# Performance work log

Measured on AMD Instinct MI355X. Metric: run time of the kernel, lower is better.

Reference implementation:

```python
import jax, jax.numpy as jnp
import numpy as np
from jax import lax

K = 31          # mip_kernel
P_LO, P_HI = 0.01, 0.99
ALPHA = 0.15
MU = 10.0
PD_ITERS = 30
TAU = 0.125
SIG = 0.125
THETA = 1.0
EPS = 1e-6


def _max_pool(x, k):
    # torch F.max_pool2d with stride=1, padding=k//2 pads with -inf
    p = k // 2
    return lax.reduce_window(
        x, -jnp.inf, lax.max,
        window_dimensions=(1, 1, k, k),
        window_strides=(1, 1, 1, 1),
        padding=[(0, 0), (0, 0), (p, p), (p, p)])


def _forward_grad(u):
    # forward differences, zero-padded on the far edge (same shape as u)
    dx = jnp.pad(u[..., :, 1:] - u[..., :, :-1], ((0, 0), (0, 0), (0, 0), (0, 1)))
    dy = jnp.pad(u[..., 1:, :] - u[..., :-1, :], ((0, 0), (0, 0), (0, 1), (0, 0)))
    return dx, dy


def _divergence(px, py):
    div_x = px - jnp.pad(px[..., :, :-1], ((0, 0), (0, 0), (0, 0), (1, 0)))
    div_y = py - jnp.pad(py[..., :-1, :], ((0, 0), (0, 0), (1, 0), (0, 0)))
    return div_x + div_y


def _robust_normalize(x):
    B = x.shape[0]
    flat = x.reshape(B, -1)
    lo = jnp.quantile(flat, P_LO, axis=1).reshape(B, 1, 1, 1)
    hi = jnp.quantile(flat, P_HI, axis=1).reshape(B, 1, 1, 1)
    return jnp.clip((x - lo) / (hi - lo + EPS), 0.0, 1.0)


def setup_inputs() -> dict:
    key = jax.random.key(0)
    Iy = jax.random.uniform(key, (16, 3, 512, 512), dtype=jnp.float32)
    return {"Iy": Iy}


def reference(Iy):
    B = Iy.shape[0]
    R, G, Bc = Iy[:, 0:1], Iy[:, 1:2], Iy[:, 2:3]

    Rmax = _max_pool(R, K)
    GBmax = jnp.maximum(_max_pool(G, K), _max_pool(Bc, K))
    Dmip_abs = jnp.abs(Rmax - GBmax)

    N_hat = _robust_normalize(Dmip_abs + R)

    dxh, dyh = _forward_grad(N_hat)
    grad_mag = jnp.sqrt(dxh * dxh + dyh * dyh + EPS)
    # sigma_mode == 'median' -> per-image median of grad magnitude
    sigma = jnp.quantile(grad_mag.reshape(B, -1), 0.5, axis=1).reshape(B, 1, 1, 1)
    sigma = jnp.maximum(sigma, EPS)

    Wx = 1.0 + MU * jnp.exp(-jnp.abs(dxh) / sigma)
    Wy = 1.0 + MU * jnp.exp(-jnp.abs(dyh) / sigma)

    def step(carry, _):
        u, u_bar, px, py = carry
        dx, dy = _forward_grad(u_bar)
        px = jnp.clip(px + SIG * dx, -ALPHA * Wx, ALPHA * Wx)
        py = jnp.clip(py + SIG * dy, -ALPHA * Wy, ALPHA * Wy)
        div_p = _divergence(px, py)
        v = u + TAU * div_p
        u_new = (v + TAU * N_hat) / (1.0 + TAU)
        u_bar = u_new + THETA * (u_new - u)
        return (u_new, u_bar, px, py), None

    z = jnp.zeros_like(N_hat)
    (u, _, _, _), _ = lax.scan(step, (N_hat, N_hat, z, z), None, length=PD_ITERS)
    return jnp.clip(u, 0.0, 1.0)
```

## Files before the change

kernel.cpp:

```cpp
#include <hip/hip_runtime.h>
#include <hip/hip_bf16.h>
#include <hip/hip_fp16.h>
#include <math.h>

#define NPIX   262144
#define NP     4194304
#define NBINS  8192
#define HSUB   16
#define RB     8
#define SIG    0.125f
#define TAUC   0.125f
#define ALPHAC 0.15f
#define MUC    10.0f
#define EPSC   1e-6f
#define NEGINF -3.4e38f
#define IVT    (1.0f / (1.0f + TAUC))

__device__ __forceinline__ void cvt8h(float4 raw, float* d) {
    const __half2* h = (const __half2*)&raw;
#pragma unroll
    for (int j = 0; j < 4; ++j) {
        float2 f = __half22float2(h[j]);
        d[2 * j] = f.x; d[2 * j + 1] = f.y;
    }
}
__device__ __forceinline__ void ld8h(const __half* p, float* d) {
    cvt8h(*(const float4*)p, d);
}
__device__ __forceinline__ float4 pk8h(const float* s) {
    float4 r; __half2* h = (__half2*)&r;
#pragma unroll
    for (int j = 0; j < 4; ++j) h[j] = __floats2half2_rn(s[2 * j], s[2 * j + 1]);
    return r;
}
__device__ __forceinline__ float bnd(float d, float inv) {
    return ALPHAC * (1.f + MUC * __expf(-fabsf(d) * inv));
}
__device__ __forceinline__ float clmp(float v, float b) {
    return fminf(fmaxf(v, -b), b);
}


__global__ __launch_bounds__(512) void hpass3_k(const float* __restrict__ Iy,
                                                __half* __restrict__ H) {
    __shared__ float rowbuf[8][512];
    __shared__ float PB[8][512];
    __shared__ float SB[8][512];
    int tid = threadIdx.x;
    int plane = blockIdx.y;
    int y0 = blockIdx.x * 8;

#pragma unroll
    for (int q = 0; q < 2; ++q) {
        int idx = q * 512 + tid;
        int r = idx >> 7;
        int x4 = (idx & 127) << 2;
        float4 v;
        if (plane < 16) {
            v = *(const float4*)(Iy + (size_t)(plane * 3) * NPIX + (size_t)(y0 + r) * 512 + x4);
        } else {
            int b = plane - 16;
            float4 g = *(const float4*)(Iy + ((size_t)(b * 3) + 1) * NPIX + (size_t)(y0 + r) * 512 + x4);
            float4 bb = *(const float4*)(Iy + ((size_t)(b * 3) + 2) * NPIX + (size_t)(y0 + r) * 512 + x4);
            v = make_float4(fmaxf(g.x, bb.x), fmaxf(g.y, bb.y), fmaxf(g.z, bb.z), fmaxf(g.w, bb.w));
        }
        *(float4*)(&rowbuf[r][x4]) = v;
    }
    __syncthreads();

    if (tid < 272) {
        int type = tid / 136;
        int rem = tid % 136;
        int r = rem / 17;
        int seg = rem % 17;
        int s0 = seg * 31;
        if (type == 0) {
            float run = rowbuf[r][s0];
            PB[r][s0] = run;
            for (int j = 1; j < 31; ++j) {
                int idx = s0 + j;
                if (idx < 512) { run = fmaxf(run, rowbuf[r][idx]); PB[r][idx] = run; }
            }
        } else {
            int s1 = min(s0 + 30, 511);
            float run = rowbuf[r][s1];
            SB[r][s1] = run;
            for (int j = s1 - 1; j >= s0; --j) { run = fmaxf(run, rowbuf[r][j]); SB[r][j] = run; }
        }
    }
    __syncthreads();

    int x = tid, a = x - 15, bc = x + 15;
#pragma unroll
    for (int r = 0; r < 8; ++r) {
        float o;
        if (a < 0)        o = PB[r][bc];
        else if (bc > 511) o = fmaxf(SB[r][a], PB[r][511]);
        else              o = fmaxf(SB[r][a], PB[r][bc]);
        H[(size_t)plane * NPIX + (size_t)(y0 + r) * 512 + x] = __float2half_rn(o);
    }
}

__global__ __launch_bounds__(64) void vpassC_k(const __half* __restrict__ H,
                                               const float* __restrict__ Iy,
                                               __half* __restrict__ xb) {
    int x = blockIdx.x * 64 + threadIdx.x;
    int b = blockIdx.z;
    const __half* inR = H + (size_t)b * NPIX;
    const __half* inM = H + (size_t)(16 + b) * NPIX;
    const float* IyR = Iy + (size_t)(b * 3) * NPIX;
    __half*      out = xb + (size_t)b * NPIX;
    int c0 = blockIdx.y * 2;

    float SprevR[31], SprevM[31];
    if (c0 > 0) {
        int s0 = (c0 - 1) * 31;
        float vR[31], vM[31];
#pragma unroll
        for (int j = 0; j < 31; ++j) {
            vR[j] = __half2float(inR[(size_t)(s0 + j) * 512 + x]);
            vM[j] = __half2float(inM[(size_t)(s0 + j) * 512 + x]);
        }
        float aR = NEGINF, aM = NEGINF;
#pragma unroll
        for (int j = 30; j >= 0; --j) {
            aR = fmaxf(aR, vR[j]); SprevR[j] = aR;
            aM = fmaxf(aM, vM[j]); SprevM[j] = aM;
        }
    } else {
#pragma unroll
        for (int j = 0; j < 31; ++j) { SprevR[j] = NEGINF; SprevM[j] = NEGINF; }
    }

    int send = min(c0 + 1, 16);
    for (int s = c0; s <= send; ++s) {
        int s0 = s * 31;
        float vR[31], vM[31];
#pragma unroll
        for (int j = 0; j < 31; ++j) {
            bool ok = (s0 + j < 512);
            vR[j] = ok ? __half2float(inR[(size_t)(s0 + j) * 512 + x]) : NEGINF;
            vM[j] = ok ? __half2float(inM[(size_t)(s0 + j) * 512 + x]) : NEGINF;
        }
        float ScurR[31], ScurM[31];
        float aR = NEGINF, aM = NEGINF;
#pragma unroll
        for (int j = 30; j >= 0; --j) {
            aR = fmaxf(aR, vR[j]); ScurR[j] = aR;
            aM = fmaxf(aM, vM[j]); ScurM[j] = aM;
        }
        float PR = NEGINF, PM = NEGINF;
#pragma unroll
        for (int r = 0; r < 31; ++r) {
            PR = fmaxf(PR, vR[r]);
            PM = fmaxf(PM, vM[r]);
            int i = s0 + r - 15;
            if (i >= 0 && i <= 511) {
                int a = s0 - 30 + r;
                float oR, oM;
                if (a < 0) { oR = PR; oM = PM; }
                else {
                    float SvR = (r == 30) ? ScurR[0] : SprevR[r + 1];
                    float SvM = (r == 30) ? ScurM[0] : SprevM[r + 1];
                    oR = fmaxf(SvR, PR);
                    oM = fmaxf(SvM, PM);
                }
                out[(size_t)i * 512 + x] =
                    __float2half_rn(fabsf(oR - oM) + IyR[(size_t)i * 512 + x]);
            }
        }
#pragma unroll
        for (int j = 0; j < 31; ++j) { SprevR[j] = ScurR[j]; SprevM[j] = ScurM[j]; }
    }
}


__global__ __launch_bounds__(1024) void hist2_k(const __half* __restrict__ v,
                                                int* __restrict__ hist) {
    __shared__ int lh[NBINS];
    int s = blockIdx.x, b = blockIdx.y, tid = threadIdx.x;
    for (int i = tid; i < NBINS; i += 1024) lh[i] = 0;
    __syncthreads();
    const __half* p = v + (size_t)b * NPIX + (size_t)s * (NPIX / HSUB);
    for (int i = tid; i < NPIX / HSUB; i += 1024) {
        int bin = (int)(__half2float(p[i]) * (NBINS * 0.5f));
        bin = min(max(bin, 0), NBINS - 1);
        atomicAdd(&lh[bin], 1);
    }
    __syncthreads();
    for (int i = tid; i < NBINS; i += 1024) {
        int c = lh[i];
        if (c) atomicAdd(&hist[b * NBINS + i], c);
    }
}

__global__ __launch_bounds__(1024) void gradhisth_k(const __half* __restrict__ nh,
                                                    int* __restrict__ hist) {
    __shared__ int lh[NBINS];
    int s = blockIdx.x, b = blockIdx.y, tid = threadIdx.x;
    for (int i = tid; i < NBINS; i += 1024) lh[i] = 0;
    __syncthreads();
    const __half* p = nh + (size_t)b * NPIX;
    int base = s * (NPIX / HSUB);
    for (int ii = tid; ii < NPIX / HSUB; ii += 1024) {
        int i = base + ii;
        float c = __half2float(p[i]);
        int x = i & 511, y = i >> 9;
        float dx = (x < 511) ? __half2float(p[i + 1])   - c : 0.f;
        float dy = (y < 511) ? __half2float(p[i + 512]) - c : 0.f;
        float gm = sqrtf(dx * dx + dy * dy + EPSC);
        int bin = (int)(gm * (NBINS * 0.5f));
        bin = min(max(bin, 0), NBINS - 1);
        atomicAdd(&lh[bin], 1);
    }
    __syncthreads();
    for (int i = tid; i < NBINS; i += 1024) {
        int c = lh[i];
        if (c) atomicAdd(&hist[b * NBINS + i], c);
    }
}

__global__ __launch_bounds__(1024) void quant2_k(const int* __restrict__ hist,
                                                 float* __restrict__ scal,
                                                 float q0, float q1, int s0, int s1) {
    __shared__ int csum[1025];
    __shared__ int wsum[16];
    int b = blockIdx.x, tid = threadIdx.x;
    const int* h = hist + b * NBINS;
    int s = 0;
#pragma unroll
    for (int j = 0; j < NBINS / 1024; ++j) s += h[tid * (NBINS / 1024) + j];

    int lane = tid & 63, wave = tid >> 6;
    int v = s;
#pragma unroll
    for (int off = 1; off < 64; off <<= 1) {
        int n = __shfl_up(v, off, 64);
        if (lane >= off) v += n;
    }
    if (lane == 63) wsum[wave] = v;
    __syncthreads();
    if (wave == 0 && lane < 16) {
        int w = wsum[lane];
#pragma unroll
        for (int off = 1; off < 16; off <<= 1) {
            int n = __shfl_up(w, off, 64);
            if (lane >= off) w += n;
        }
        wsum[lane] = w;
    }
    __syncthreads();
    int incl = v + (wave > 0 ? wsum[wave - 1] : 0);
    csum[tid + 1] = incl;
    if (tid == 0) csum[0] = 0;
    __syncthreads();

#pragma unroll
    for (int pass = 0; pass < 2; ++pass) {
        int slot = pass ? s1 : s0;
        if (slot < 0) continue;
        float q = pass ? q1 : q0;
        float t = q * (float)(NPIX - 1);
        if ((float)csum[tid] <= t && (float)csum[tid + 1] > t) {
            const int per = NBINS / 1024;
            int cb = csum[tid];
            int bin = tid * per;
            int hv = 1;
            for (int j = 0; j < per; ++j) {
                hv = h[tid * per + j];
                if ((float)(cb + hv) > t) { bin = tid * per + j; break; }
                cb += hv;
            }
            float k = t - (float)cb;
            scal[b * 4 + slot] = ((float)bin + (k + 0.5f) / (float)hv) * (2.0f / NBINS);
        }
    }
}

__global__ __launch_bounds__(256) void nhat2h_k(const __half* __restrict__ xb,
                                                const float* __restrict__ scal,
                                                __half* __restrict__ nhh) {
    size_t i = ((size_t)blockIdx.x * 256 + threadIdx.x) * 8;
    int b = (int)(i >> 18);
    float lo = scal[b * 4 + 0], hi = scal[b * 4 + 1];
    float inv = 1.0f / (hi - lo + EPSC);
    float v[8]; ld8h(xb + i, v);
    float a[8];
#pragma unroll
    for (int j = 0; j < 8; ++j)
        a[j] = fminf(fmaxf((v[j] - lo) * inv, 0.f), 1.f);
    *(float4*)(nhh + i) = pk8h(a);
}

__global__ __launch_bounds__(256) void pdf2_k(const __half* __restrict__ u,
                                              const __half* __restrict__ up,
                                              const __half* __restrict__ pxO,
                                              const __half* __restrict__ pyO,
                                              __half* __restrict__ pxN,
                                              __half* __restrict__ pyN,
                                              const __half* __restrict__ nh,
                                              const float* __restrict__ scal,
                                              __half* __restrict__ u1g,
                                              __half* __restrict__ u2g,
                                              float* __restrict__ outF,
                                              int last) {
    __shared__ __align__(16) char smem[75776];
    float  (*ubar0)[512] = (float (*)[512])smem;
    __half (*u1l)[512]   = (__half(*)[512])smem;
    __half (*u0l)[512]   = (__half(*)[512])(smem + 10240);
    __half (*nhl)[512]   = (__half(*)[512])(smem + 24576);
    __half (*px1)[512]   = (__half(*)[512])(smem + 36864);
    __half (*py1)[512]   = (__half(*)[512])(smem + 47104);
    __half (*px2l)[512]  = (__half(*)[512])(smem + 58368);
    __half (*py2l)[512]  = (__half(*)[512])(smem + 66560);

    int tid = threadIdx.x;
    int sub = tid >> 6, lane = tid & 63, x0 = lane * 8;
    int y0 = blockIdx.x * RB;
    int b = blockIdx.y;
    size_t plane = (size_t)b * NPIX;
    float sgm = fmaxf(scal[b * 4 + 2], EPSC);
    float inv = 1.0f / sgm;
    const float4 z4 = make_float4(0.f, 0.f, 0.f, 0.f);

    for (int i = sub; i < 12; i += 4) {
        int g = y0 - 2 + i;
        if (g >= 0 && g < 512) {
            size_t off = plane + (size_t)g * 512 + x0;
            float uu[8], pp[8];
            ld8h(u + off, uu); ld8h(up + off, pp);
#pragma unroll
            for (int j = 0; j < 8; ++j) ubar0[i][x0 + j] = 2.f * uu[j] - pp[j];
            *(float4*)&nhl[i][x0] = *(const float4*)(nh + off);
        } else {
            *(float4*)&ubar0[i][x0]     = z4;
            *(float4*)&ubar0[i][x0 + 4] = z4;
            *(float4*)&nhl[i][x0] = z4;
        }
    }
    __syncthreads();

    for (int c = sub; c < 11; c += 4) {
        int g = y0 - 2 + c;
        if (g >= 0 && g < 512) {
            size_t off = plane + (size_t)g * 512 + x0;
            float nhc[8], nhd[8], ubc[8], ubd[8];
            ld8h(&nhl[c][x0], nhc);
            ld8h(&nhl[c + 1][x0], nhd);
            float t0[8], t1[8];
            float4 a0 = *(float4*)&ubar0[c][x0];
            float4 a1 = *(float4*)&ubar0[c][x0 + 4];
            t0[0]=a0.x; t0[1]=a0.y; t0[2]=a0.z; t0[3]=a0.w;
            t0[4]=a1.x; t0[5]=a1.y; t0[6]=a1.z; t0[7]=a1.w;
            float4 b0 = *(float4*)&ubar0[c + 1][x0];
            float4 b1 = *(float4*)&ubar0[c + 1][x0 + 4];
            t1[0]=b0.x; t1[1]=b0.y; t1[2]=b0.z; t1[3]=b0.w;
            t1[4]=b1.x; t1[5]=b1.y; t1[6]=b1.z; t1[7]=b1.w;
#pragma unroll
            for (int j = 0; j < 8; ++j) { ubc[j] = t0[j]; ubd[j] = t1[j]; }
            float nhRr = (lane < 63) ? __half2float(nhl[c][x0 + 8]) : 0.f;
            float ubRr = (lane < 63) ? ubar0[c][x0 + 8] : 0.f;
            bool rD = (g < 511);
            float py0v[8]; ld8h(pyO + off, py0v);
            float pyv[8];
#pragma unroll
            for (int j = 0; j < 8; ++j) {
                float by = bnd(rD ? (nhd[j] - nhc[j]) : 0.f, inv);
                float dy = rD ? (ubd[j] - ubc[j]) : 0.f;
                pyv[j] = clmp(py0v[j] + SIG * dy, by);
            }
            *(float4*)&py1[c][x0] = pk8h(pyv);
            if (c >= 1) {
                float px0v[8]; ld8h(pxO + off, px0v);
                float pxv[8];
#pragma unroll
                for (int j = 0; j < 8; ++j) {
                    int x = x0 + j;
                    bool xok = (x < 511);
                    float nhr = (j < 7) ? nhc[j + 1] : nhRr;
                    float ubr = (j < 7) ? ubc[j + 1] : ubRr;
                    float bx = bnd(xok ? (nhr - nhc[j]) : 0.f, inv);
                    float dx = xok ? (ubr - ubc[j]) : 0.f;
                    pxv[j] = clmp(px0v[j] + SIG * dx, bx);
                }
                *(float4*)&px1[c - 1][x0] = pk8h(pxv);
            }
        } else {
            *(float4*)&py1[c][x0] = z4;
            if (c >= 1) *(float4*)&px1[c - 1][x0] = z4;
        }
    }
    __syncthreads();

    for (int a = sub; a < 10; a += 4) {
        int g = y0 - 1 + a;
        if (g >= 0 && g < 512) {
            size_t off = plane + (size_t)g * 512 + x0;
            float4 u0raw = *(const float4*)(u + off);
            float u0v[8]; cvt8h(u0raw, u0v);
            float nhc[8];  ld8h(&nhl[a + 1][x0], nhc);
            float px1c[8]; ld8h(&px1[a][x0], px1c);
            float py1c[8]; ld8h(&py1[a + 1][x0], py1c);
            float py1u[8]; ld8h(&py1[a][x0], py1u);
            float pxl = (x0 > 0) ? __half2float(px1[a][x0 - 1]) : 0.f;
            bool gU = (g > 0);
            float uv[8];
#pragma unroll
            for (int j = 0; j < 8; ++j) {
                int x = x0 + j;
                float left = (x > 0) ? ((j > 0) ? px1c[j - 1] : pxl) : 0.f;
                float div = px1c[j] - left + py1c[j] - (gU ? py1u[j] : 0.f);
                uv[j] = (u0v[j] + TAUC * div + TAUC * nhc[j]) * IVT;
            }
            float4 packed = pk8h(uv);
            *(float4*)&u1l[a][x0] = packed;
            *(float4*)&u0l[a][x0] = u0raw;
            if (!last && g >= y0 && g < y0 + RB) *(float4*)(u1g + off) = packed;
        } else {
            *(float4*)&u1l[a][x0] = z4;
            *(float4*)&u0l[a][x0] = z4;
        }
    }
    __syncthreads();

    for (int e = sub; e < 9; e += 4) {
        int g = y0 - 1 + e;
        if (g >= 0) {
            size_t off = plane + (size_t)g * 512 + x0;
            float u1c[8], u0c[8], u1d[8], u0d[8];
            ld8h(&u1l[e][x0], u1c);     ld8h(&u0l[e][x0], u0c);
            ld8h(&u1l[e + 1][x0], u1d); ld8h(&u0l[e + 1][x0], u0d);
            float nhc[8], nhd[8];
            ld8h(&nhl[e + 1][x0], nhc); ld8h(&nhl[e + 2][x0], nhd);
            float ubc[8], ubd[8];
#pragma unroll
            for (int j = 0; j < 8; ++j) {
                ubc[j] = 2.f * u1c[j] - u0c[j];
                ubd[j] = 2.f * u1d[j] - u0d[j];
            }
            float ubRr = (lane < 63) ? (2.f * __half2float(u1l[e][x0 + 8]) - __half2float(u0l[e][x0 + 8])) : 0.f;
            float nhRr = (lane < 63) ? __half2float(nhl[e + 1][x0 + 8]) : 0.f;
            bool rD = (g < 511);
            float py1c[8]; ld8h(&py1[e + 1][x0], py1c);
            float pyv[8];
#pragma unroll
            for (int j = 0; j < 8; ++j) {
                float by = bnd(rD ? (nhd[j] - nhc[j]) : 0.f, inv);
                float dy = rD ? (ubd[j] - ubc[j]) : 0.f;
                pyv[j] = clmp(py1c[j] + SIG * dy, by);
            }
            float4 pyp = pk8h(pyv);
            *(float4*)&py2l[e][x0] = pyp;
            if (!last && g >= y0) *(float4*)(pyN + off) = pyp;
            if (e >= 1) {
                float px1c[8]; ld8h(&px1[e][x0], px1c);
                float pxv[8];
#pragma unroll
                for (int j = 0; j < 8; ++j) {
                    int x = x0 + j;
                    bool xok = (x < 511);
                    float nhr = (j < 7) ? nhc[j + 1] : nhRr;
                    float ubr = (j < 7) ? ubc[j + 1] : ubRr;
                    float bx = bnd(xok ? (nhr - nhc[j]) : 0.f, inv);
                    float dx = xok ? (ubr - ubc[j]) : 0.f;
                    pxv[j] = clmp(px1c[j] + SIG * dx, bx);
                }
                float4 pxp = pk8h(pxv);
                *(float4*)&px2l[e - 1][x0] = pxp;
                if (!last) *(float4*)(pxN + off) = pxp;
            }
        } else {
            *(float4*)&py2l[e][x0] = z4;
        }
    }
    __syncthreads();

    for (int d = sub; d < 8; d += 4) {
        int g = y0 + d;
        size_t off = plane + (size_t)g * 512 + x0;
        float px2c[8]; ld8h(&px2l[d][x0], px2c);
        float py2c[8]; ld8h(&py2l[d + 1][x0], py2c);
        float py2u[8]; ld8h(&py2l[d][x0], py2u);
        float pxl = (x0 > 0) ? __half2float(px2l[d][x0 - 1]) : 0.f;
        float u1c[8]; ld8h(&u1l[d + 1][x0], u1c);
        float nhc[8]; ld8h(&nhl[d + 2][x0], nhc);
        bool gU = (g > 0);
        float uv[8];
#pragma unroll
        for (int j = 0; j < 8; ++j) {
            int x = x0 + j;
            float left = (x > 0) ? ((j > 0) ? px2c[j - 1] : pxl) : 0.f;
            float div = px2c[j] - left + py2c[j] - (gU ? py2u[j] : 0.f);
            uv[j] = (u1c[j] + TAUC * div + TAUC * nhc[j]) * IVT;
        }
        if (last) {
            float4 o0, o1;
            o0.x = fminf(fmaxf(uv[0], 0.f), 1.f);
            o0.y = fminf(fmaxf(uv[1], 0.f), 1.f);
            o0.z = fminf(fmaxf(uv[2], 0.f), 1.f);
            o0.w = fminf(fmaxf(uv[3], 0.f), 1.f);
            o1.x = fminf(fmaxf(uv[4], 0.f), 1.f);
            o1.y = fminf(fmaxf(uv[5], 0.f), 1.f);
            o1.z = fminf(fmaxf(uv[6], 0.f), 1.f);
            o1.w = fminf(fmaxf(uv[7], 0.f), 1.f);
            *(float4*)(outF + off)     = o0;
            *(float4*)(outF + off + 4) = o1;
        } else {
            *(float4*)(u2g + off) = pk8h(uv);
        }
    }
}

extern "C" void kernel_launch(void* const* d_in, const int* in_sizes, int n_in,
                              void* d_out, int out_size, void* d_ws, size_t ws_size,
                              hipStream_t stream) {
    const float* Iy = (const float*)d_in[0];
    float* out = (float*)d_out;

    dim3 hist_g(HSUB, 16);
    dim3 pd2_g(512 / RB, 16);

    __half* hb  = (__half*)d_ws;
    __half* nhh = hb;
    __half* HA  = hb + (size_t)NP;
    __half* HB  = hb + (size_t)2 * NP;
    __half* HC  = hb + (size_t)3 * NP;
    __half* HD  = hb + (size_t)4 * NP;
    __half* pxA = hb + (size_t)5 * NP;
    __half* pyA = hb + (size_t)6 * NP;
    __half* pxB = hb + (size_t)7 * NP;
    __half* pyB = hb + (size_t)8 * NP;
    __half* xbh = hb + (size_t)9 * NP;
    __half* Hh  = hb + (size_t)10 * NP;
    int*    hist = (int*)(hb + (size_t)12 * NP);
    float*  scal = (float*)(hist + 16 * NBINS);

    hpass3_k<<<dim3(64, 32), dim3(512), 0, stream>>>(Iy, Hh);
    vpassC_k<<<dim3(8, 9, 16), dim3(64), 0, stream>>>(Hh, Iy, xbh);

    hipMemsetAsync(hist, 0, 16 * NBINS * sizeof(int), stream);
    hist2_k<<<hist_g, 1024, 0, stream>>>(xbh, hist);
    quant2_k<<<16, 1024, 0, stream>>>(hist, scal, 0.01f, 0.99f, 0, 1);
    nhat2h_k<<<NP / 2048, 256, 0, stream>>>(xbh, scal, nhh);

    hipMemsetAsync(hist, 0, 16 * NBINS * sizeof(int), stream);
    gradhisth_k<<<hist_g, 1024, 0, stream>>>(nhh, hist);
    quant2_k<<<16, 1024, 0, stream>>>(hist, scal, 0.5f, 0.5f, 2, -1);
    hipMemsetAsync(pxA, 0, (size_t)2 * NP * sizeof(__half), stream);

    const __half* ucur = nhh;
    const __half* uprev = nhh;
    __half* pxs[2] = {pxA, pxB};
    __half* pys[2] = {pyA, pyB};
    for (int k = 0; k < 15; ++k) {
        int cur = k & 1;
        __half* u1o = (k & 1) ? HC : HA;
        __half* u2o = (k & 1) ? HD : HB;
        pdf2_k<<<pd2_g, 256, 0, stream>>>(ucur, uprev,
                                          pxs[cur], pys[cur],
                                          pxs[cur ^ 1], pys[cur ^ 1],
                                          nhh, scal, u1o, u2o, out,
                                          (k == 14) ? 1 : 0);
        uprev = u1o;
        ucur = u2o;
    }
}
```

Measured before the change: 510.7 us.

## Split vertical max-pool into per-plane kernel plus combine; cache u0 in shared memory

```diff
diff --git a/kernel.cpp b/kernel.cpp
--- a/kernel.cpp
+++ b/kernel.cpp
@@ -101,77 +101,62 @@
     }
 }
 
-__global__ __launch_bounds__(64) void vpassC_k(const __half* __restrict__ H,
-                                               const float* __restrict__ Iy,
-                                               __half* __restrict__ xb) {
+__global__ __launch_bounds__(64) void vpass2h_k(const __half* __restrict__ H,
+                                                __half* __restrict__ V) {
     int x = blockIdx.x * 64 + threadIdx.x;
-    int b = blockIdx.z;
-    const __half* inR = H + (size_t)b * NPIX;
-    const __half* inM = H + (size_t)(16 + b) * NPIX;
-    const float* IyR = Iy + (size_t)(b * 3) * NPIX;
-    __half*      out = xb + (size_t)b * NPIX;
-    int c0 = blockIdx.y * 2;
-
-    float SprevR[31], SprevM[31];
-    if (c0 > 0) {
-        int s0 = (c0 - 1) * 31;
-        float vR[31], vM[31];
-#pragma unroll
-        for (int j = 0; j < 31; ++j) {
-            vR[j] = __half2float(inR[(size_t)(s0 + j) * 512 + x]);
-            vM[j] = __half2float(inM[(size_t)(s0 + j) * 512 + x]);
-        }
-        float aR = NEGINF, aM = NEGINF;
-#pragma unroll
-        for (int j = 30; j >= 0; --j) {
-            aR = fmaxf(aR, vR[j]); SprevR[j] = aR;
-            aM = fmaxf(aM, vM[j]); SprevM[j] = aM;
-        }
+    int s = blockIdx.y;
+    const __half* in = H + (size_t)blockIdx.z * NPIX;
+    __half*      out = V + (size_t)blockIdx.z * NPIX;
+    int s0 = s * 31;
+
+    float Sprev[31];
+    if (s > 0) {
+        int p0 = s0 - 31;
+        float v[31];
+#pragma unroll
+        for (int j = 0; j < 31; ++j) v[j] = __half2float(in[(size_t)(p0 + j) * 512 + x]);
+        float acc = NEGINF;
+#pragma unroll
+        for (int j = 30; j >= 0; --j) { acc = fmaxf(acc, v[j]); Sprev[j] = acc; }
     } else {
 #pragma unroll
-        for (int j = 0; j < 31; ++j) { SprevR[j] = NEGINF; SprevM[j] = NEGINF; }
-    }
-
-    int send = min(c0 + 1, 16);
-    for (int s = c0; s <= send; ++s) {
-        int s0 = s * 31;
-        float vR[31], vM[31];
-#pragma unroll
-        for (int j = 0; j < 31; ++j) {
-            bool ok = (s0 + j < 512);
-            vR[j] = ok ? __half2float(inR[(size_t)(s0 + j) * 512 + x]) : NEGINF;
-            vM[j] = ok ? __half2float(inM[(size_t)(s0 + j) * 512 + x]) : NEGINF;
-        }
-        float ScurR[31], ScurM[31];
-        float aR = NEGINF, aM = NEGINF;
-#pragma unroll
-        for (int j = 30; j >= 0; --j) {
-            aR = fmaxf(aR, vR[j]); ScurR[j] = aR;
-            aM = fmaxf(aM, vM[j]); ScurM[j] = aM;
-        }
-        float PR = NEGINF, PM = NEGINF;
-#pragma unroll
-        for (int r = 0; r < 31; ++r) {
-            PR = fmaxf(PR, vR[r]);
-            PM = fmaxf(PM, vM[r]);
-            int i = s0 + r - 15;
-            if (i >= 0 && i <= 511) {
-                int a = s0 - 30 + r;
-                float oR, oM;
-                if (a < 0) { oR = PR; oM = PM; }
-                else {
-                    float SvR = (r == 30) ? ScurR[0] : SprevR[r + 1];
-                    float SvM = (r == 30) ? ScurM[0] : SprevM[r + 1];
-                    oR = fmaxf(SvR, PR);
-                    oM = fmaxf(SvM, PM);
-                }
-                out[(size_t)i * 512 + x] =
-                    __float2half_rn(fabsf(oR - oM) + IyR[(size_t)i * 512 + x]);
-            }
-        }
-#pragma unroll
-        for (int j = 0; j < 31; ++j) { SprevR[j] = ScurR[j]; SprevM[j] = ScurM[j]; }
-    }
+        for (int j = 0; j < 31; ++j) Sprev[j] = NEGINF;
+    }
+
+    float P = NEGINF;
+#pragma unroll
+    for (int r = 0; r < 31; ++r) {
+        float vv = (s0 + r < 512) ? __half2float(in[(size_t)(s0 + r) * 512 + x]) : NEGINF;
+        P = fmaxf(P, vv);
+        int i = s0 + r - 15;
+        if (i >= 0 && i <= 511) {
+            int a = s0 + r - 30;
+            float o;
+            if (a < 0)       o = P;
+            else if (r == 30) o = P;
+            else              o = fmaxf(Sprev[r + 1], P);
+            out[(size_t)i * 512 + x] = __float2half_rn(o);
+        }
+    }
+}
+
+__global__ __launch_bounds__(256) void combineh_k(const __half* __restrict__ V,
+                                                  const float* __restrict__ Iy,
+                                                  __half* __restrict__ xb) {
+    size_t i = ((size_t)blockIdx.x * 256 + threadIdx.x) * 8;
+    int b = (int)(i >> 18);
+    size_t off = i & (NPIX - 1);
+    float vr[8], vm[8];
+    ld8h(V + (size_t)b * NPIX + off, vr);
+    ld8h(V + (size_t)(16 + b) * NPIX + off, vm);
+    const float* R = Iy + (size_t)(b * 3) * NPIX + off;
+    float4 r0 = *(const float4*)R;
+    float4 r1 = *(const float4*)(R + 4);
+    float rr[8] = {r0.x, r0.y, r0.z, r0.w, r1.x, r1.y, r1.z, r1.w};
+    float a[8];
+#pragma unroll
+    for (int j = 0; j < 8; ++j) a[j] = fabsf(vr[j] - vm[j]) + rr[j];
+    *(float4*)(xb + i) = pk8h(a);
 }
 
 
@@ -304,15 +289,15 @@
                                               __half* __restrict__ u2g,
                                               float* __restrict__ outF,
                                               int last) {
-    __shared__ __align__(16) char smem[75776];
-    float  (*ubar0)[512] = (float (*)[512])smem;
-    __half (*u1l)[512]   = (__half(*)[512])smem;
-    __half (*u0l)[512]   = (__half(*)[512])(smem + 10240);
-    __half (*nhl)[512]   = (__half(*)[512])(smem + 24576);
-    __half (*px1)[512]   = (__half(*)[512])(smem + 36864);
-    __half (*py1)[512]   = (__half(*)[512])(smem + 47104);
-    __half (*px2l)[512]  = (__half(*)[512])(smem + 58368);
-    __half (*py2l)[512]  = (__half(*)[512])(smem + 66560);
+    __shared__ __align__(16) char smem[76800];
+    __half (*ubar0h)[512] = (__half(*)[512])smem;
+    __half (*py2l)[512]   = (__half(*)[512])smem;
+    __half (*u0l)[512]    = (__half(*)[512])(smem + 12288);
+    __half (*nhl)[512]    = (__half(*)[512])(smem + 24576);
+    __half (*px1)[512]    = (__half(*)[512])(smem + 36864);
+    __half (*py1)[512]    = (__half(*)[512])(smem + 47104);
+    __half (*u1l)[512]    = (__half(*)[512])(smem + 58368);
+    __half (*px2l)[512]   = (__half(*)[512])(smem + 68608);
 
     int tid = threadIdx.x;
     int sub = tid >> 6, lane = tid & 63, x0 = lane * 8;
@@ -327,14 +312,17 @@
         int g = y0 - 2 + i;
         if (g >= 0 && g < 512) {
             size_t off = plane + (size_t)g * 512 + x0;
-            float uu[8], pp[8];
-            ld8h(u + off, uu); ld8h(up + off, pp);
-#pragma unroll
-            for (int j = 0; j < 8; ++j) ubar0[i][x0 + j] = 2.f * uu[j] - pp[j];
+            float4 uraw = *(const float4*)(u + off);
+            float uu[8], pp[8], ub[8];
+            cvt8h(uraw, uu); ld8h(up + off, pp);
+#pragma unroll
+            for (int j = 0; j < 8; ++j) ub[j] = 2.f * uu[j] - pp[j];
+            *(float4*)&ubar0h[i][x0] = pk8h(ub);
+            *(float4*)&u0l[i][x0] = uraw;
             *(float4*)&nhl[i][x0] = *(const float4*)(nh + off);
         } else {
-            *(float4*)&ubar0[i][x0]     = z4;
-            *(float4*)&ubar0[i][x0 + 4] = z4;
+            *(float4*)&ubar0h[i][x0] = z4;
+            *(float4*)&u0l[i][x0] = z4;
             *(float4*)&nhl[i][x0] = z4;
         }
     }
@@ -347,19 +335,10 @@
             float nhc[8], nhd[8], ubc[8], ubd[8];
             ld8h(&nhl[c][x0], nhc);
             ld8h(&nhl[c + 1][x0], nhd);
-            float t0[8], t1[8];
-            float4 a0 = *(float4*)&ubar0[c][x0];
-            float4 a1 = *(float4*)&ubar0[c][x0 + 4];
-            t0[0]=a0.x; t0[1]=a0.y; t0[2]=a0.z; t0[3]=a0.w;
-            t0[4]=a1.x; t0[5]=a1.y; t0[6]=a1.z; t0[7]=a1.w;
-            float4 b0 = *(float4*)&ubar0[c + 1][x0];
-            float4 b1 = *(float4*)&ubar0[c + 1][x0 + 4];
-            t1[0]=b0.x; t1[1]=b0.y; t1[2]=b0.z; t1[3]=b0.w;
-            t1[4]=b1.x; t1[5]=b1.y; t1[6]=b1.z; t1[7]=b1.w;
-#pragma unroll
-            for (int j = 0; j < 8; ++j) { ubc[j] = t0[j]; ubd[j] = t1[j]; }
+            ld8h(&ubar0h[c][x0], ubc);
+            ld8h(&ubar0h[c + 1][x0], ubd);
             float nhRr = (lane < 63) ? __half2float(nhl[c][x0 + 8]) : 0.f;
-            float ubRr = (lane < 63) ? ubar0[c][x0 + 8] : 0.f;
+            float ubRr = (lane < 63) ? __half2float(ubar0h[c][x0 + 8]) : 0.f;
             bool rD = (g < 511);
             float py0v[8]; ld8h(pyO + off, py0v);
             float pyv[8];
@@ -395,9 +374,7 @@
     for (int a = sub; a < 10; a += 4) {
         int g = y0 - 1 + a;
         if (g >= 0 && g < 512) {
-            size_t off = plane + (size_t)g * 512 + x0;
-            float4 u0raw = *(const float4*)(u + off);
-            float u0v[8]; cvt8h(u0raw, u0v);
+            float u0v[8]; ld8h(&u0l[a + 1][x0], u0v);
             float nhc[8];  ld8h(&nhl[a + 1][x0], nhc);
             float px1c[8]; ld8h(&px1[a][x0], px1c);
             float py1c[8]; ld8h(&py1[a + 1][x0], py1c);
@@ -414,11 +391,12 @@
             }
             float4 packed = pk8h(uv);
             *(float4*)&u1l[a][x0] = packed;
-            *(float4*)&u0l[a][x0] = u0raw;
-            if (!last && g >= y0 && g < y0 + RB) *(float4*)(u1g + off) = packed;
+            if (!last && g >= y0 && g < y0 + RB) {
+                size_t off = plane + (size_t)g * 512 + x0;
+                *(float4*)(u1g + off) = packed;
+            }
         } else {
             *(float4*)&u1l[a][x0] = z4;
-            *(float4*)&u0l[a][x0] = z4;
         }
     }
     __syncthreads();
@@ -428,8 +406,8 @@
         if (g >= 0) {
             size_t off = plane + (size_t)g * 512 + x0;
             float u1c[8], u0c[8], u1d[8], u0d[8];
-            ld8h(&u1l[e][x0], u1c);     ld8h(&u0l[e][x0], u0c);
-            ld8h(&u1l[e + 1][x0], u1d); ld8h(&u0l[e + 1][x0], u0d);
+            ld8h(&u1l[e][x0], u1c);     ld8h(&u0l[e + 1][x0], u0c);
+            ld8h(&u1l[e + 1][x0], u1d); ld8h(&u0l[e + 2][x0], u0d);
             float nhc[8], nhd[8];
             ld8h(&nhl[e + 1][x0], nhc); ld8h(&nhl[e + 2][x0], nhd);
             float ubc[8], ubd[8];
@@ -438,7 +416,7 @@
                 ubc[j] = 2.f * u1c[j] - u0c[j];
                 ubd[j] = 2.f * u1d[j] - u0d[j];
             }
-            float ubRr = (lane < 63) ? (2.f * __half2float(u1l[e][x0 + 8]) - __half2float(u0l[e][x0 + 8])) : 0.f;
+            float ubRr = (lane < 63) ? (2.f * __half2float(u1l[e][x0 + 8]) - __half2float(u0l[e + 1][x0 + 8])) : 0.f;
             float nhRr = (lane < 63) ? __half2float(nhl[e + 1][x0 + 8]) : 0.f;
             bool rD = (g < 511);
             float py1c[8]; ld8h(&py1[e + 1][x0], py1c);
@@ -532,11 +510,13 @@
     __half* pyB = hb + (size_t)8 * NP;
     __half* xbh = hb + (size_t)9 * NP;
     __half* Hh  = hb + (size_t)10 * NP;
+    __half* Vh  = hb + (size_t)1 * NP;
     int*    hist = (int*)(hb + (size_t)12 * NP);
     float*  scal = (float*)(hist + 16 * NBINS);
 
     hpass3_k<<<dim3(64, 32), dim3(512), 0, stream>>>(Iy, Hh);
-    vpassC_k<<<dim3(8, 9, 16), dim3(64), 0, stream>>>(Hh, Iy, xbh);
+    vpass2h_k<<<dim3(8, 17, 32), dim3(64), 0, stream>>>(Hh, Vh);
+    combineh_k<<<NP / 2048, 256, 0, stream>>>(Vh, Iy, xbh);
 
     hipMemsetAsync(hist, 0, 16 * NBINS * sizeof(int), stream);
     hist2_k<<<hist_g, 1024, 0, stream>>>(xbh, hist);
```

Result: faster. 485.1 us (-5.0%).
